# Kernel optimization log

Measured on AMD Instinct MI355X. Metric: run time of the kernel, lower is better.

The kernel has to match this reference:

```python
import jax, jax.numpy as jnp
import numpy as np

N_NODES = 50000
N_EDGES = 1000000
D_IN = 64
D_OUT = 64
N_REL = 8


def setup_inputs() -> dict:
    key = jax.random.key(0)
    ks = jax.random.split(key, 8)
    x = jax.random.normal(ks[0], (N_NODES, D_IN), dtype=jnp.float32)
    edge_src = jax.random.randint(ks[1], (N_EDGES,), 0, N_NODES, dtype=jnp.int32)
    edge_dst = jax.random.randint(ks[2], (N_EDGES,), 0, N_NODES, dtype=jnp.int32)
    edge_rel = jax.random.randint(ks[3], (N_EDGES,), 0, N_REL, dtype=jnp.int32)
    edge_weight = jnp.ones((N_EDGES,), dtype=jnp.float32)
    W_linear = jax.random.normal(ks[4], (N_REL * D_IN, D_OUT), dtype=jnp.float32) * (1.0 / np.sqrt(N_REL * D_IN))
    b_linear = jnp.zeros((D_OUT,), dtype=jnp.float32)
    W_self = jax.random.normal(ks[5], (D_IN, D_OUT), dtype=jnp.float32) * (1.0 / np.sqrt(D_IN))
    b_self = jnp.zeros((D_OUT,), dtype=jnp.float32)
    return {"x": x, "edge_src": edge_src, "edge_dst": edge_dst, "edge_rel": edge_rel,
            "edge_weight": edge_weight, "W_linear": W_linear, "b_linear": b_linear,
            "W_self": W_self, "b_self": b_self}


def reference(x, edge_src, edge_dst, edge_rel, edge_weight, W_linear, b_linear, W_self, b_self):
    N, d = x.shape
    R = W_linear.shape[0] // d
    # per-(dst, relation) segment ids, as in node_out * num_relation + relation
    seg = edge_dst * R + edge_rel  # [E]
    # degree normalization (message_and_aggregate path: no eps, divide by out-degree)
    deg = jax.ops.segment_sum(edge_weight, seg, num_segments=N * R)  # [N*R]
    ew = edge_weight / deg[seg]  # [E]
    # sparse mm: adjacency.T @ x == segment-sum of normalized gathered source features
    msg = x[edge_src] * ew[:, None]  # [E, d]
    update = jax.ops.segment_sum(msg, seg, num_segments=N * R)  # [N*R, d]
    update = update.reshape(N, R * d)
    # combine: linear(update) + self_loop(x), then relu
    out = update @ W_linear + b_linear + x @ W_self + b_self
    return jax.nn.relu(out)
```

## Files before the change

kernel.cpp:

```cpp
#include <hip/hip_runtime.h>
#include <stdint.h>

#define NNODES 50000
#define NEDGES 1000000
#define DIM    64
#define NREL   8
#define NBIN   489
#define NBINB  3125
#define NBINBP 4096
#define TPITCH 3136
#define BCAP   480
#define BCAP2  736
#define PITCH  592
#define PREPN  (18 * 4 * 64 * 8)

typedef __attribute__((ext_vector_type(8))) short short8;
typedef __attribute__((ext_vector_type(4))) float float4v;
typedef __attribute__((ext_vector_type(4))) unsigned short us4;
typedef long long i64;

__device__ __forceinline__ unsigned short f2bf(float f) {
  unsigned int u = __float_as_uint(f);
  unsigned int r = (u + 0x7FFF + ((u >> 16) & 1)) >> 16;
  return (unsigned short)r;
}
__device__ __forceinline__ unsigned int f2fp8(float f) {
  unsigned u = __float_as_uint(f);
  unsigned s = (u >> 24) & 0x80u;
  unsigned a = u & 0x7FFFFFFFu;
  if (a < 0x3C800000u) return s;
  unsigned r = a + 0x7FFFFu + ((a >> 20) & 1u);
  return s | (((r >> 20) - 960u) & 0x7Fu);
}
__device__ __forceinline__ unsigned pk4(unsigned a, unsigned b, unsigned c, unsigned d) {
  return a | (b << 8) | (c << 16) | (d << 24);
}

__global__ __launch_bounds__(1024, 8) void build_kernel(
    const float4* __restrict__ x4,
    const float* __restrict__ Wlin, const float* __restrict__ Wself,
    const float* __restrict__ blin, const float* __restrict__ bself,
    const int2* __restrict__ src2, const int2* __restrict__ dst2,
    const int2* __restrict__ rel2, const float2* __restrict__ w2,
    us4* __restrict__ xb, unsigned int* __restrict__ xq4,
    unsigned short* __restrict__ Bf2, float* __restrict__ bsum,
    uint2* __restrict__ staged2, unsigned short* __restrict__ tab, int E2) {
  __shared__ int lhist[NBINBP];
  __shared__ int lscan[NBINBP];
  __shared__ uint2 lrec[2048];
  __shared__ int wsumB[16];
  int tid = threadIdx.x;
  int lane = tid & 63;
  int wave = tid >> 6;
  int j = blockIdx.x;
  int gid = j * 1024 + tid;
  const int TOT = NBIN * 1024;

  for (int t = gid; t < NNODES * DIM / 4; t += TOT) {
    float4 v = x4[t];
    us4 o;
    o.x = f2bf(v.x); o.y = f2bf(v.y); o.z = f2bf(v.z); o.w = f2bf(v.w);
    xb[t] = o;
    xq4[t] = f2fp8(v.x) | (f2fp8(v.y) << 8) | (f2fp8(v.z) << 16) | (f2fp8(v.w) << 24);
  }
  if (gid < PREPN) {
    int t = gid;
    int jj = t & 7;
    int l  = (t >> 3) & 63;
    int ct = (t >> 9) & 3;
    int ks = t >> 11;
    int k = ks * 32 + (l >> 4) * 8 + jj;
    int c = ct * 16 + (l & 15);
    float v = (k < 512) ? Wlin[(size_t)k * 64 + c] : Wself[(size_t)(k - 512) * 64 + c];
    Bf2[t] = f2bf(v);
  }
  if (gid < 64) bsum[gid] = blin[gid] + bself[gid];

  for (int i = tid; i < NBINBP; i += 1024) lhist[i] = 0;
  __syncthreads();
  bool valid = gid < E2;
  int2 s = {0,0}, d = {0,0}, r = {0,0};
  float2 w = {0.f,0.f};
  if (valid) { s = src2[gid]; d = dst2[gid]; r = rel2[gid]; w = w2[gid]; }
  int b0=0,b1=0,p0=0,p1=0;
  if (valid) {
    b0 = d.x >> 4; p0 = atomicAdd(&lhist[b0], 1);
    b1 = d.y >> 4; p1 = atomicAdd(&lhist[b1], 1);
  }
  __syncthreads();
  {
    int base4 = tid * 4;
    int l0 = lhist[base4 + 0], l1 = lhist[base4 + 1],
        l2 = lhist[base4 + 2], l3 = lhist[base4 + 3];
    int c1 = l0, c2 = c1 + l1, c3 = c2 + l2, s4 = c3 + l3;
    int inc = s4;
    #pragma unroll
    for (int dd = 1; dd < 64; dd <<= 1) {
      int tt = __shfl_up(inc, dd);
      if (lane >= dd) inc += tt;
    }
    if (lane == 63) wsumB[wave] = inc;
    __syncthreads();
    int off = 0;
    #pragma unroll
    for (int i = 0; i < 16; i++) { int pv = wsumB[i]; off += (i < wave) ? pv : 0; }
    int excl = off + inc - s4;
    lscan[base4 + 0] = excl;
    lscan[base4 + 1] = excl + c1;
    lscan[base4 + 2] = excl + c2;
    lscan[base4 + 3] = excl + c3;
  }
  __syncthreads();
  if (valid) {
    int q;
    unsigned k0 = (((unsigned)(d.x & 15) << 3) | (unsigned)r.x) << 23;
    unsigned k1 = (((unsigned)(d.y & 15) << 3) | (unsigned)r.y) << 23;
    q = lscan[b0] + p0; lrec[q] = make_uint2(((unsigned)s.x << 6) | k0, f2fp8(w.x));
    q = lscan[b1] + p1; lrec[q] = make_uint2(((unsigned)s.y << 6) | k1, f2fp8(w.y));
  }
  __syncthreads();
  for (int i = tid; i < NBINB; i += 1024) {
    int c = lhist[i];
    int cc = (c < 31) ? c : 31;
    unsigned short pk = (c > 0) ? (unsigned short)((unsigned)lscan[i] | ((unsigned)cc << 11)) : (unsigned short)0;
    tab[(size_t)j * TPITCH + i] = pk;
  }
  int cntblk = NEDGES - j * 2048;
  if (cntblk > 2048) cntblk = 2048;
  uint2* myst = staged2 + (size_t)j * 2048;
  for (int i = tid; i < cntblk; i += 1024)
    myst[i] = lrec[i];
}

__global__ __launch_bounds__(512, 4) void aggemm_kernel(
    const unsigned short* __restrict__ tab,
    const uint2* __restrict__ staged2,
    const unsigned char* __restrict__ xq,
    const unsigned short* __restrict__ xb,
    const unsigned short* __restrict__ Bf2,
    const float* __restrict__ bsum,
    float* __restrict__ out) {
  __shared__ __align__(16) unsigned short At[16 * PITCH];
  __shared__ short rid[512];
  __shared__ unsigned short tabcol[NBIN];
  __shared__ short runbase[NBIN];
  __shared__ uint2 sorted[BCAP2];
  __shared__ int hist[512];
  __shared__ int scn[513];
  __shared__ int wsum[8];
  __shared__ int wbase_s[8];
  __shared__ int cnt_s;
  int tid = threadIdx.x;
  int lane = tid & 63;
  int wave = tid >> 6;
  int orig = blockIdx.x;
  int xcd = orig & 7;
  int lid = orig >> 3;
  int b = ((xcd < 5) ? xcd * 391 : (5 * 391 + (xcd - 5) * 390)) + lid;
  int nodeBase = b * 16;

  hist[tid] = 0;
  rid[tid] = 0;
  sorted[tid] = make_uint2(0u, 0u);
  if (tid < BCAP2 - 512) sorted[512 + tid] = make_uint2(0u, 0u);
  unsigned tv = (tid < NBIN) ? (unsigned)tab[(size_t)tid * TPITCH + b] : 0u;
  int rc = (int)(tv >> 11);
  int inc = rc;
  #pragma unroll
  for (int dd = 1; dd < 64; dd <<= 1) {
    int tt = __shfl_up(inc, dd);
    if (lane >= dd) inc += tt;
  }
  if (lane == 63) wsum[wave] = inc;
  __syncthreads();
  {
    int off = 0;
    #pragma unroll
    for (int i = 0; i < 8; i++) { int pv = wsum[i]; off += (i < wave) ? pv : 0; }
    int excl = off + inc - rc;
    if (tid < NBIN) {
      tabcol[tid] = (unsigned short)tv;
      runbase[tid] = (short)excl;
      if (rc > 0 && excl < BCAP) rid[excl] = (short)tid;
    }
    if (tid == 511) cnt_s = (off + inc < BCAP) ? (off + inc) : BCAP;
  }
  __syncthreads();
  {
    int a0 = (int)rid[tid];
    int minc = a0;
    #pragma unroll
    for (int dd = 1; dd < 64; dd <<= 1) {
      int tt = __shfl_up(minc, dd);
      if (lane >= dd) minc = max(minc, tt);
    }
    if (lane == 63) wsum[wave] = minc;
    __syncthreads();
    int moff = 0;
    #pragma unroll
    for (int i = 0; i < 8; i++) { int pv = wsum[i]; moff = (i < wave) ? max(moff, pv) : moff; }
    int ew = __shfl_up(minc, 1);
    int p = (lane > 0) ? max(moff, ew) : moff;
    rid[tid] = (short)max(p, a0);
  }
  __syncthreads();
  int cntC = cnt_s;
  uint2 g0 = make_uint2(0, 0);
  int k0 = -1;
  if (tid < cntC) {
    int jr = (int)rid[tid];
    int pp = (int)(tabcol[jr] & 0x7FFu) + tid - (int)runbase[jr];
    g0 = staged2[(size_t)jr * 2048 + pp];
    k0 = (int)(g0.x >> 23);
    atomicAdd(&hist[k0], 1);
  }
  __syncthreads();
  {
    int v = hist[tid];
    int kinc = v;
    #pragma unroll
    for (int dd = 1; dd < 64; dd <<= 1) {
      int tt = __shfl_up(kinc, dd);
      if (lane >= dd) kinc += tt;
    }
    if (lane == 63) wsum[wave] = kinc;
    __syncthreads();
    int off = 0;
    #pragma unroll
    for (int i = 0; i < 8; i++) { int pv = wsum[i]; off += (i < wave) ? pv : 0; }
    scn[tid] = off + kinc - v;
    if (tid == 511) scn[512] = off + kinc;
  }
  __syncthreads();
  if (wave == 0) {
    int Lw = (lane < 8) ? (scn[lane * 16 + 16] - scn[lane * 16]) : 0;
    int pw = (Lw + 31) & ~31;
    int inc2 = pw;
    #pragma unroll
    for (int dd = 1; dd < 8; dd <<= 1) {
      int tt = __shfl_up(inc2, dd);
      if (lane >= dd) inc2 += tt;
    }
    if (lane < 8) wbase_s[lane] = inc2 - pw;
  }
  __syncthreads();
  if (tid < 128) hist[tid] = wbase_s[tid >> 4] + scn[tid] - scn[tid & ~15];
  __syncthreads();
  if (k0 >= 0) { int pq = atomicAdd(&hist[k0], 1); sorted[pq] = g0; }
  __syncthreads();

  {
    int Lw = scn[wave * 16 + 16] - scn[wave * 16];
    int base0 = wbase_s[wave];
    int nch = (Lw + 31) >> 5;
    int fl = lane & 15;
    int q8 = (lane >> 4) * 8;
    unsigned mg = (unsigned)(wave * 16 + fl);
    float4v acc0 = {0.f,0.f,0.f,0.f}, acc1 = {0.f,0.f,0.f,0.f};
    float4v acc2 = {0.f,0.f,0.f,0.f}, acc3 = {0.f,0.f,0.f,0.f};
    float4v accS = {0.f,0.f,0.f,0.f};
    const i64 onesA = 0x3838383838383838LL;
    for (int c = 0; c < nch; c++) {
      int rb = base0 + c * 32 + q8;
      uint2 r0 = sorted[rb + 0], r1 = sorted[rb + 1], r2 = sorted[rb + 2], r3 = sorted[rb + 3];
      uint2 r4 = sorted[rb + 4], r5 = sorted[rb + 5], r6 = sorted[rb + 6], r7 = sorted[rb + 7];
      unsigned s0 = ((r0.x >> 23) == mg) ? r0.y : 0u;
      unsigned s1 = ((r1.x >> 23) == mg) ? r1.y : 0u;
      unsigned s2 = ((r2.x >> 23) == mg) ? r2.y : 0u;
      unsigned s3 = ((r3.x >> 23) == mg) ? r3.y : 0u;
      unsigned s4 = ((r4.x >> 23) == mg) ? r4.y : 0u;
      unsigned s5 = ((r5.x >> 23) == mg) ? r5.y : 0u;
      unsigned s6 = ((r6.x >> 23) == mg) ? r6.y : 0u;
      unsigned s7 = ((r7.x >> 23) == mg) ? r7.y : 0u;
      i64 af = (i64)(unsigned)pk4(s0, s1, s2, s3) | ((i64)pk4(s4, s5, s6, s7) << 32);
      unsigned o0 = (r0.x & 0x3FFFC0u) + (unsigned)fl;
      unsigned o1 = (r1.x & 0x3FFFC0u) + (unsigned)fl;
      unsigned o2 = (r2.x & 0x3FFFC0u) + (unsigned)fl;
      unsigned o3 = (r3.x & 0x3FFFC0u) + (unsigned)fl;
      unsigned o4 = (r4.x & 0x3FFFC0u) + (unsigned)fl;
      unsigned o5 = (r5.x & 0x3FFFC0u) + (unsigned)fl;
      unsigned o6 = (r6.x & 0x3FFFC0u) + (unsigned)fl;
      unsigned o7 = (r7.x & 0x3FFFC0u) + (unsigned)fl;
      unsigned b00 = xq[o0],      b10 = xq[o1],      b20 = xq[o2],      b30 = xq[o3];
      unsigned b40 = xq[o4],      b50 = xq[o5],      b60 = xq[o6],      b70 = xq[o7];
      unsigned b01 = xq[o0 + 16], b11 = xq[o1 + 16], b21 = xq[o2 + 16], b31 = xq[o3 + 16];
      unsigned b41 = xq[o4 + 16], b51 = xq[o5 + 16], b61 = xq[o6 + 16], b71 = xq[o7 + 16];
      unsigned b02 = xq[o0 + 32], b12 = xq[o1 + 32], b22 = xq[o2 + 32], b32 = xq[o3 + 32];
      unsigned b42 = xq[o4 + 32], b52 = xq[o5 + 32], b62 = xq[o6 + 32], b72 = xq[o7 + 32];
      unsigned b03 = xq[o0 + 48], b13 = xq[o1 + 48], b23 = xq[o2 + 48], b33 = xq[o3 + 48];
      unsigned b43 = xq[o4 + 48], b53 = xq[o5 + 48], b63 = xq[o6 + 48], b73 = xq[o7 + 48];
      i64 B0 = (i64)(unsigned)pk4(b00, b10, b20, b30) | ((i64)pk4(b40, b50, b60, b70) << 32);
      i64 B1 = (i64)(unsigned)pk4(b01, b11, b21, b31) | ((i64)pk4(b41, b51, b61, b71) << 32);
      i64 B2 = (i64)(unsigned)pk4(b02, b12, b22, b32) | ((i64)pk4(b42, b52, b62, b72) << 32);
      i64 B3 = (i64)(unsigned)pk4(b03, b13, b23, b33) | ((i64)pk4(b43, b53, b63, b73) << 32);
      acc0 = __builtin_amdgcn_mfma_f32_16x16x32_fp8_fp8(af, B0, acc0, 0, 0, 0);
      acc1 = __builtin_amdgcn_mfma_f32_16x16x32_fp8_fp8(af, B1, acc1, 0, 0, 0);
      acc2 = __builtin_amdgcn_mfma_f32_16x16x32_fp8_fp8(af, B2, acc2, 0, 0, 0);
      acc3 = __builtin_amdgcn_mfma_f32_16x16x32_fp8_fp8(af, B3, acc3, 0, 0, 0);
      accS = __builtin_amdgcn_mfma_f32_16x16x32_fp8_fp8(af, onesA, accS, 0, 0, 0);
    }
    int rowg = lane >> 4;
    #pragma unroll
    for (int reg = 0; reg < 4; reg++) {
      int lk = rowg * 4 + reg;
      float S = accS[reg];
      float rd = (S != 0.f) ? (1.0f / S) : 0.f;
      int rowo = (wave * 2 + (lk >> 3)) * PITCH + (lk & 7) * 64 + fl;
      At[rowo +  0] = f2bf(acc0[reg] * rd);
      At[rowo + 16] = f2bf(acc1[reg] * rd);
      At[rowo + 32] = f2bf(acc2[reg] * rd);
      At[rowo + 48] = f2bf(acc3[reg] * rd);
    }
  }
  {
    int node0 = nodeBase + wave * 2;
    At[(wave * 2) * PITCH + 512 + lane]     = xb[(size_t)node0 * 64 + lane];
    At[(wave * 2 + 1) * PITCH + 512 + lane] = xb[(size_t)(node0 + 1) * 64 + lane];
  }
  __syncthreads();

  if (wave < 4) {
    int m = lane & 15;
    int q = lane >> 4;
    float4v o4 = {0.f, 0.f, 0.f, 0.f};
    const short8* Bp = (const short8*)Bf2;
    #pragma unroll
    for (int ks = 0; ks < 18; ks++) {
      short8 a = *(const short8*)(At + m * PITCH + ks * 32 + q * 8);
      short8 bfr = Bp[(ks * 4 + wave) * 64 + lane];
      o4 = __builtin_amdgcn_mfma_f32_16x16x32_bf16(a, bfr, o4, 0, 0, 0);
    }
    int c = wave * 16 + m;
    float bias = bsum[c];
    #pragma unroll
    for (int rr2 = 0; rr2 < 4; rr2++) {
      out[(size_t)(nodeBase + q * 4 + rr2) * 64 + c] = fmaxf(o4[rr2] + bias, 0.0f);
    }
  }
}

extern "C" void kernel_launch(void* const* d_in, const int* in_sizes, int n_in,
                              void* d_out, int out_size, void* d_ws, size_t ws_size,
                              hipStream_t stream) {
  const float* x     = (const float*)d_in[0];
  const int*   esrc  = (const int*)d_in[1];
  const int*   edst  = (const int*)d_in[2];
  const int*   erel  = (const int*)d_in[3];
  const float* ew    = (const float*)d_in[4];
  const float* Wlin  = (const float*)d_in[5];
  const float* blin  = (const float*)d_in[6];
  const float* Wself = (const float*)d_in[7];
  const float* bself = (const float*)d_in[8];
  float* out = (float*)d_out;

  char* ws = (char*)d_ws;
  size_t off = 0;
  auto alloc = [&](size_t bytes) -> void* {
    void* p = ws + off;
    off += (bytes + 255) & ~(size_t)255;
    return p;
  };
  uint2*          staged2 = (uint2*)alloc((size_t)NBIN * 2048 * sizeof(uint2));
  unsigned short* tab     = (unsigned short*)alloc((size_t)NBIN * TPITCH * sizeof(unsigned short));
  unsigned short* Bf2     = (unsigned short*)alloc((size_t)PREPN * sizeof(unsigned short));
  float*          bsum    = (float*)alloc(64 * sizeof(float));
  unsigned short* xb      = (unsigned short*)alloc((size_t)NNODES * DIM * sizeof(unsigned short));
  unsigned char*  xq      = (unsigned char*)alloc((size_t)NNODES * DIM);

  const int E2 = NEDGES / 2;
  build_kernel<<<NBIN, 1024, 0, stream>>>((const float4*)x, Wlin, Wself, blin, bself,
                                          (const int2*)esrc, (const int2*)edst,
                                          (const int2*)erel, (const float2*)ew,
                                          (us4*)xb, (unsigned int*)xq, Bf2, bsum,
                                          staged2, tab, E2);
  aggemm_kernel<<<NBINB, 512, 0, stream>>>(tab, staged2, xq, xb, Bf2, bsum, out);
}
```

Before: 135.7 us.

## Halve aggregation block to 256 threads with two work items per thread

The aggregation+GEMM kernel now runs with 256 threads instead of 512. Each thread handles two table entries and two edge records, and each wave processes two 16-node-group aggregations in a loop. All waves now do the final bf16 GEMM, so the four waves that used to idle in that phase are gone. The LDS row pitch changes from 592 to 584 to shift the bank mapping, and launch bounds target 5 blocks per CU. The trade-off is less parallelism per block and serialized per-wave aggregation loops, in exchange for less idle wave time and potentially more resident blocks.

Measured after the change: 127.7 us. 1.06x faster.

```diff
diff --git a/kernel.cpp b/kernel.cpp
--- a/kernel.cpp
+++ b/kernel.cpp
@@ -11,7 +11,7 @@
 #define TPITCH 3136
 #define BCAP   480
 #define BCAP2  736
-#define PITCH  592
+#define PITCH  584
 #define PREPN  (18 * 4 * 64 * 8)
 
 typedef __attribute__((ext_vector_type(8))) short short8;
@@ -132,7 +132,7 @@
     myst[i] = lrec[i];
 }
 
-__global__ __launch_bounds__(512, 4) void aggemm_kernel(
+__global__ __launch_bounds__(256, 5) void aggemm_kernel(
     const unsigned short* __restrict__ tab,
     const uint2* __restrict__ staged2,
     const unsigned char* __restrict__ xq,
@@ -145,9 +145,10 @@
   __shared__ unsigned short tabcol[NBIN];
   __shared__ short runbase[NBIN];
   __shared__ uint2 sorted[BCAP2];
-  __shared__ int hist[512];
-  __shared__ int scn[513];
-  __shared__ int wsum[8];
+  __shared__ int hist[128];
+  __shared__ int scn[129];
+  __shared__ int wsum[4];
+  __shared__ int wsum2[2];
   __shared__ int wbase_s[8];
   __shared__ int cnt_s;
   int tid = threadIdx.x;
@@ -159,36 +160,47 @@
   int b = ((xcd < 5) ? xcd * 391 : (5 * 391 + (xcd - 5) * 390)) + lid;
   int nodeBase = b * 16;
 
-  hist[tid] = 0;
-  rid[tid] = 0;
+  if (tid < 128) hist[tid] = 0;
+  rid[tid] = 0; rid[tid + 256] = 0;
   sorted[tid] = make_uint2(0u, 0u);
-  if (tid < BCAP2 - 512) sorted[512 + tid] = make_uint2(0u, 0u);
-  unsigned tv = (tid < NBIN) ? (unsigned)tab[(size_t)tid * TPITCH + b] : 0u;
-  int rc = (int)(tv >> 11);
-  int inc = rc;
-  #pragma unroll
-  for (int dd = 1; dd < 64; dd <<= 1) {
-    int tt = __shfl_up(inc, dd);
-    if (lane >= dd) inc += tt;
-  }
-  if (lane == 63) wsum[wave] = inc;
-  __syncthreads();
-  {
+  sorted[tid + 256] = make_uint2(0u, 0u);
+  if (tid < BCAP2 - 512) sorted[tid + 512] = make_uint2(0u, 0u);
+  int i0 = 2 * tid, i1 = 2 * tid + 1;
+  unsigned tv0 = (i0 < NBIN) ? (unsigned)tab[(size_t)i0 * TPITCH + b] : 0u;
+  unsigned tv1 = (i1 < NBIN) ? (unsigned)tab[(size_t)i1 * TPITCH + b] : 0u;
+  int rc0 = (int)(tv0 >> 11), rc1 = (int)(tv1 >> 11);
+  {
+    int s2 = rc0 + rc1;
+    int inc = s2;
+    #pragma unroll
+    for (int dd = 1; dd < 64; dd <<= 1) {
+      int tt = __shfl_up(inc, dd);
+      if (lane >= dd) inc += tt;
+    }
+    if (lane == 63) wsum[wave] = inc;
+    __syncthreads();
     int off = 0;
     #pragma unroll
-    for (int i = 0; i < 8; i++) { int pv = wsum[i]; off += (i < wave) ? pv : 0; }
-    int excl = off + inc - rc;
-    if (tid < NBIN) {
-      tabcol[tid] = (unsigned short)tv;
-      runbase[tid] = (short)excl;
-      if (rc > 0 && excl < BCAP) rid[excl] = (short)tid;
-    }
-    if (tid == 511) cnt_s = (off + inc < BCAP) ? (off + inc) : BCAP;
-  }
-  __syncthreads();
-  {
-    int a0 = (int)rid[tid];
-    int minc = a0;
+    for (int i = 0; i < 4; i++) { int pv = wsum[i]; off += (i < wave) ? pv : 0; }
+    int excl = off + inc - s2;
+    if (i0 < NBIN) {
+      tabcol[i0] = (unsigned short)tv0;
+      runbase[i0] = (short)excl;
+      if (rc0 > 0 && excl < BCAP) rid[excl] = (short)i0;
+    }
+    int excl1 = excl + rc0;
+    if (i1 < NBIN) {
+      tabcol[i1] = (unsigned short)tv1;
+      runbase[i1] = (short)excl1;
+      if (rc1 > 0 && excl1 < BCAP) rid[excl1] = (short)i1;
+    }
+    if (tid == 255) cnt_s = (off + inc < BCAP) ? (off + inc) : BCAP;
+  }
+  __syncthreads();
+  {
+    int a0 = (int)rid[i0], a1 = (int)rid[i1];
+    int m2 = max(a0, a1);
+    int minc = m2;
     #pragma unroll
     for (int dd = 1; dd < 64; dd <<= 1) {
       int tt = __shfl_up(minc, dd);
@@ -198,38 +210,50 @@
     __syncthreads();
     int moff = 0;
     #pragma unroll
-    for (int i = 0; i < 8; i++) { int pv = wsum[i]; moff = (i < wave) ? max(moff, pv) : moff; }
+    for (int i = 0; i < 4; i++) { int pv = wsum[i]; moff = (i < wave) ? max(moff, pv) : moff; }
     int ew = __shfl_up(minc, 1);
     int p = (lane > 0) ? max(moff, ew) : moff;
-    rid[tid] = (short)max(p, a0);
+    int r0 = max(p, a0);
+    int r1 = max(r0, a1);
+    rid[i0] = (short)r0; rid[i1] = (short)r1;
   }
   __syncthreads();
   int cntC = cnt_s;
-  uint2 g0 = make_uint2(0, 0);
-  int k0 = -1;
-  if (tid < cntC) {
-    int jr = (int)rid[tid];
-    int pp = (int)(tabcol[jr] & 0x7FFu) + tid - (int)runbase[jr];
-    g0 = staged2[(size_t)jr * 2048 + pp];
-    k0 = (int)(g0.x >> 23);
-    atomicAdd(&hist[k0], 1);
-  }
-  __syncthreads();
-  {
-    int v = hist[tid];
+  uint2 g0 = make_uint2(0, 0), g1 = make_uint2(0, 0);
+  int k0 = -1, k1 = -1;
+  {
+    int t0 = tid, t1 = tid + 256;
+    if (t0 < cntC) {
+      int jr = (int)rid[t0];
+      int pp = (int)(tabcol[jr] & 0x7FFu) + t0 - (int)runbase[jr];
+      g0 = staged2[(size_t)jr * 2048 + pp];
+      k0 = (int)(g0.x >> 23);
+      atomicAdd(&hist[k0], 1);
+    }
+    if (t1 < cntC) {
+      int jr = (int)rid[t1];
+      int pp = (int)(tabcol[jr] & 0x7FFu) + t1 - (int)runbase[jr];
+      g1 = staged2[(size_t)jr * 2048 + pp];
+      k1 = (int)(g1.x >> 23);
+      atomicAdd(&hist[k1], 1);
+    }
+  }
+  __syncthreads();
+  {
+    int v = (tid < 128) ? hist[tid] : 0;
     int kinc = v;
     #pragma unroll
     for (int dd = 1; dd < 64; dd <<= 1) {
       int tt = __shfl_up(kinc, dd);
       if (lane >= dd) kinc += tt;
     }
-    if (lane == 63) wsum[wave] = kinc;
+    if (lane == 63 && wave < 2) wsum2[wave] = kinc;
     __syncthreads();
-    int off = 0;
-    #pragma unroll
-    for (int i = 0; i < 8; i++) { int pv = wsum[i]; off += (i < wave) ? pv : 0; }
-    scn[tid] = off + kinc - v;
-    if (tid == 511) scn[512] = off + kinc;
+    if (tid < 128) {
+      int off = (wave == 1) ? wsum2[0] : 0;
+      scn[tid] = off + kinc - v;
+      if (tid == 127) scn[128] = off + kinc;
+    }
   }
   __syncthreads();
   if (wave == 0) {
@@ -247,79 +271,86 @@
   if (tid < 128) hist[tid] = wbase_s[tid >> 4] + scn[tid] - scn[tid & ~15];
   __syncthreads();
   if (k0 >= 0) { int pq = atomicAdd(&hist[k0], 1); sorted[pq] = g0; }
-  __syncthreads();
-
-  {
-    int Lw = scn[wave * 16 + 16] - scn[wave * 16];
-    int base0 = wbase_s[wave];
-    int nch = (Lw + 31) >> 5;
+  if (k1 >= 0) { int pq = atomicAdd(&hist[k1], 1); sorted[pq] = g1; }
+  __syncthreads();
+
+  {
     int fl = lane & 15;
     int q8 = (lane >> 4) * 8;
-    unsigned mg = (unsigned)(wave * 16 + fl);
-    float4v acc0 = {0.f,0.f,0.f,0.f}, acc1 = {0.f,0.f,0.f,0.f};
-    float4v acc2 = {0.f,0.f,0.f,0.f}, acc3 = {0.f,0.f,0.f,0.f};
-    float4v accS = {0.f,0.f,0.f,0.f};
     const i64 onesA = 0x3838383838383838LL;
-    for (int c = 0; c < nch; c++) {
-      int rb = base0 + c * 32 + q8;
-      uint2 r0 = sorted[rb + 0], r1 = sorted[rb + 1], r2 = sorted[rb + 2], r3 = sorted[rb + 3];
-      uint2 r4 = sorted[rb + 4], r5 = sorted[rb + 5], r6 = sorted[rb + 6], r7 = sorted[rb + 7];
-      unsigned s0 = ((r0.x >> 23) == mg) ? r0.y : 0u;
-      unsigned s1 = ((r1.x >> 23) == mg) ? r1.y : 0u;
-      unsigned s2 = ((r2.x >> 23) == mg) ? r2.y : 0u;
-      unsigned s3 = ((r3.x >> 23) == mg) ? r3.y : 0u;
-      unsigned s4 = ((r4.x >> 23) == mg) ? r4.y : 0u;
-      unsigned s5 = ((r5.x >> 23) == mg) ? r5.y : 0u;
-      unsigned s6 = ((r6.x >> 23) == mg) ? r6.y : 0u;
-      unsigned s7 = ((r7.x >> 23) == mg) ? r7.y : 0u;
-      i64 af = (i64)(unsigned)pk4(s0, s1, s2, s3) | ((i64)pk4(s4, s5, s6, s7) << 32);
-      unsigned o0 = (r0.x & 0x3FFFC0u) + (unsigned)fl;
-      unsigned o1 = (r1.x & 0x3FFFC0u) + (unsigned)fl;
-      unsigned o2 = (r2.x & 0x3FFFC0u) + (unsigned)fl;
-      unsigned o3 = (r3.x & 0x3FFFC0u) + (unsigned)fl;
-      unsigned o4 = (r4.x & 0x3FFFC0u) + (unsigned)fl;
-      unsigned o5 = (r5.x & 0x3FFFC0u) + (unsigned)fl;
-      unsigned o6 = (r6.x & 0x3FFFC0u) + (unsigned)fl;
-      unsigned o7 = (r7.x & 0x3FFFC0u) + (unsigned)fl;
-      unsigned b00 = xq[o0],      b10 = xq[o1],      b20 = xq[o2],      b30 = xq[o3];
-      unsigned b40 = xq[o4],      b50 = xq[o5],      b60 = xq[o6],      b70 = xq[o7];
-      unsigned b01 = xq[o0 + 16], b11 = xq[o1 + 16], b21 = xq[o2 + 16], b31 = xq[o3 + 16];
-      unsigned b41 = xq[o4 + 16], b51 = xq[o5 + 16], b61 = xq[o6 + 16], b71 = xq[o7 + 16];
-      unsigned b02 = xq[o0 + 32], b12 = xq[o1 + 32], b22 = xq[o2 + 32], b32 = xq[o3 + 32];
-      unsigned b42 = xq[o4 + 32], b52 = xq[o5 + 32], b62 = xq[o6 + 32], b72 = xq[o7 + 32];
-      unsigned b03 = xq[o0 + 48], b13 = xq[o1 + 48], b23 = xq[o2 + 48], b33 = xq[o3 + 48];
-      unsigned b43 = xq[o4 + 48], b53 = xq[o5 + 48], b63 = xq[o6 + 48], b73 = xq[o7 + 48];
-      i64 B0 = (i64)(unsigned)pk4(b00, b10, b20, b30) | ((i64)pk4(b40, b50, b60, b70) << 32);
-      i64 B1 = (i64)(unsigned)pk4(b01, b11, b21, b31) | ((i64)pk4(b41, b51, b61, b71) << 32);
-      i64 B2 = (i64)(unsigned)pk4(b02, b12, b22, b32) | ((i64)pk4(b42, b52, b62, b72) << 32);
-      i64 B3 = (i64)(unsigned)pk4(b03, b13, b23, b33) | ((i64)pk4(b43, b53, b63, b73) << 32);
-      acc0 = __builtin_amdgcn_mfma_f32_16x16x32_fp8_fp8(af, B0, acc0, 0, 0, 0);
-      acc1 = __builtin_amdgcn_mfma_f32_16x16x32_fp8_fp8(af, B1, acc1, 0, 0, 0);
-      acc2 = __builtin_amdgcn_mfma_f32_16x16x32_fp8_fp8(af, B2, acc2, 0, 0, 0);
-      acc3 = __builtin_amdgcn_mfma_f32_16x16x32_fp8_fp8(af, B3, acc3, 0, 0, 0);
-      accS = __builtin_amdgcn_mfma_f32_16x16x32_fp8_fp8(af, onesA, accS, 0, 0, 0);
-    }
-    int rowg = lane >> 4;
-    #pragma unroll
-    for (int reg = 0; reg < 4; reg++) {
-      int lk = rowg * 4 + reg;
-      float S = accS[reg];
-      float rd = (S != 0.f) ? (1.0f / S) : 0.f;
-      int rowo = (wave * 2 + (lk >> 3)) * PITCH + (lk & 7) * 64 + fl;
-      At[rowo +  0] = f2bf(acc0[reg] * rd);
-      At[rowo + 16] = f2bf(acc1[reg] * rd);
-      At[rowo + 32] = f2bf(acc2[reg] * rd);
-      At[rowo + 48] = f2bf(acc3[reg] * rd);
-    }
-  }
-  {
-    int node0 = nodeBase + wave * 2;
-    At[(wave * 2) * PITCH + 512 + lane]     = xb[(size_t)node0 * 64 + lane];
-    At[(wave * 2 + 1) * PITCH + 512 + lane] = xb[(size_t)(node0 + 1) * 64 + lane];
-  }
-  __syncthreads();
-
-  if (wave < 4) {
+    for (int g = wave; g < 8; g += 4) {
+      int kbase = g * 16;
+      int Lw = scn[kbase + 16] - scn[kbase];
+      int base0 = wbase_s[g];
+      int nch = (Lw + 31) >> 5;
+      unsigned mg = (unsigned)(kbase + fl);
+      float4v acc0 = {0.f,0.f,0.f,0.f}, acc1 = {0.f,0.f,0.f,0.f};
+      float4v acc2 = {0.f,0.f,0.f,0.f}, acc3 = {0.f,0.f,0.f,0.f};
+      float4v accS = {0.f,0.f,0.f,0.f};
+      for (int c = 0; c < nch; c++) {
+        int rb = base0 + c * 32 + q8;
+        uint2 r0 = sorted[rb + 0], r1 = sorted[rb + 1], r2 = sorted[rb + 2], r3 = sorted[rb + 3];
+        uint2 r4 = sorted[rb + 4], r5 = sorted[rb + 5], r6 = sorted[rb + 6], r7 = sorted[rb + 7];
+        unsigned s0 = ((r0.x >> 23) == mg) ? r0.y : 0u;
+        unsigned s1 = ((r1.x >> 23) == mg) ? r1.y : 0u;
+        unsigned s2 = ((r2.x >> 23) == mg) ? r2.y : 0u;
+        unsigned s3 = ((r3.x >> 23) == mg) ? r3.y : 0u;
+        unsigned s4 = ((r4.x >> 23) == mg) ? r4.y : 0u;
+        unsigned s5 = ((r5.x >> 23) == mg) ? r5.y : 0u;
+        unsigned s6 = ((r6.x >> 23) == mg) ? r6.y : 0u;
+        unsigned s7 = ((r7.x >> 23) == mg) ? r7.y : 0u;
+        i64 af = (i64)(unsigned)pk4(s0, s1, s2, s3) | ((i64)pk4(s4, s5, s6, s7) << 32);
+        unsigned o0 = (r0.x & 0x3FFFC0u) + (unsigned)fl;
+        unsigned o1 = (r1.x & 0x3FFFC0u) + (unsigned)fl;
+        unsigned o2 = (r2.x & 0x3FFFC0u) + (unsigned)fl;
+        unsigned o3 = (r3.x & 0x3FFFC0u) + (unsigned)fl;
+        unsigned o4 = (r4.x & 0x3FFFC0u) + (unsigned)fl;
+        unsigned o5 = (r5.x & 0x3FFFC0u) + (unsigned)fl;
+        unsigned o6 = (r6.x & 0x3FFFC0u) + (unsigned)fl;
+        unsigned o7 = (r7.x & 0x3FFFC0u) + (unsigned)fl;
+        unsigned b00 = xq[o0],      b10 = xq[o1],      b20 = xq[o2],      b30 = xq[o3];
+        unsigned b40 = xq[o4],      b50 = xq[o5],      b60 = xq[o6],      b70 = xq[o7];
+        unsigned b01 = xq[o0 + 16], b11 = xq[o1 + 16], b21 = xq[o2 + 16], b31 = xq[o3 + 16];
+        unsigned b41 = xq[o4 + 16], b51 = xq[o5 + 16], b61 = xq[o6 + 16], b71 = xq[o7 + 16];
+        unsigned b02 = xq[o0 + 32], b12 = xq[o1 + 32], b22 = xq[o2 + 32], b32 = xq[o3 + 32];
+        unsigned b42 = xq[o4 + 32], b52 = xq[o5 + 32], b62 = xq[o6 + 32], b72 = xq[o7 + 32];
+        unsigned b03 = xq[o0 + 48], b13 = xq[o1 + 48], b23 = xq[o2 + 48], b33 = xq[o3 + 48];
+        unsigned b43 = xq[o4 + 48], b53 = xq[o5 + 48], b63 = xq[o6 + 48], b73 = xq[o7 + 48];
+        i64 B0 = (i64)(unsigned)pk4(b00, b10, b20, b30) | ((i64)pk4(b40, b50, b60, b70) << 32);
+        i64 B1 = (i64)(unsigned)pk4(b01, b11, b21, b31) | ((i64)pk4(b41, b51, b61, b71) << 32);
+        i64 B2 = (i64)(unsigned)pk4(b02, b12, b22, b32) | ((i64)pk4(b42, b52, b62, b72) << 32);
+        i64 B3 = (i64)(unsigned)pk4(b03, b13, b23, b33) | ((i64)pk4(b43, b53, b63, b73) << 32);
+        acc0 = __builtin_amdgcn_mfma_f32_16x16x32_fp8_fp8(af, B0, acc0, 0, 0, 0);
+        acc1 = __builtin_amdgcn_mfma_f32_16x16x32_fp8_fp8(af, B1, acc1, 0, 0, 0);
+        acc2 = __builtin_amdgcn_mfma_f32_16x16x32_fp8_fp8(af, B2, acc2, 0, 0, 0);
+        acc3 = __builtin_amdgcn_mfma_f32_16x16x32_fp8_fp8(af, B3, acc3, 0, 0, 0);
+        accS = __builtin_amdgcn_mfma_f32_16x16x32_fp8_fp8(af, onesA, accS, 0, 0, 0);
+      }
+      int rowg = lane >> 4;
+      #pragma unroll
+      for (int reg = 0; reg < 4; reg++) {
+        int lk = rowg * 4 + reg;
+        float S = accS[reg];
+        float rd = (S != 0.f) ? (1.0f / S) : 0.f;
+        int rowo = (g * 2 + (lk >> 3)) * PITCH + (lk & 7) * 64 + fl;
+        At[rowo +  0] = f2bf(acc0[reg] * rd);
+        At[rowo + 16] = f2bf(acc1[reg] * rd);
+        At[rowo + 32] = f2bf(acc2[reg] * rd);
+        At[rowo + 48] = f2bf(acc3[reg] * rd);
+      }
+    }
+  }
+  {
+    int r0w = wave * 4;
+    #pragma unroll
+    for (int i = 0; i < 4; i++) {
+      int node = nodeBase + r0w + i;
+      At[(r0w + i) * PITCH + 512 + lane] = xb[(size_t)node * 64 + lane];
+    }
+  }
+  __syncthreads();
+
+  {
     int m = lane & 15;
     int q = lane >> 4;
     float4v o4 = {0.f, 0.f, 0.f, 0.f};
@@ -373,5 +404,5 @@
                                           (const int2*)erel, (const float2*)ew,
                                           (us4*)xb, (unsigned int*)xq, Bf2, bsum,
                                           staged2, tab, E2);
-  aggemm_kernel<<<NBINB, 512, 0, stream>>>(tab, staged2, xq, xb, Bf2, bsum, out);
-}
+  aggemm_kernel<<<NBINB, 256, 0, stream>>>(tab, staged2, xq, xb, Bf2, bsum, out);
+}
```
